# Performance work log

Measured on AMD Instinct MI355X. Metric: run time of the kernel, lower is better.

The kernel has to match this reference:

```python
import jax, jax.numpy as jnp
import numpy as np

B, T, C, H = 2, 1024, 1024, 16
N = C // H
D_W, D_A, D_V, D_G = 64, 64, 32, 160
VOCAB = 50257


def setup_inputs() -> dict:
    key = jax.random.key(0)
    ks = iter(jax.random.split(key, 48))
    rn = lambda shape, s=1.0: jax.random.normal(next(ks), shape, dtype=jnp.float32) * s
    inp = {
        'residual': rn((B, T, C)),
        'x': rn((B, T, C)),
        'v_first': rn((B, T, C)),
        'x0': rn((B, T, C)),
        'dx0': rn((B, T, C)),
        'token_ids': jax.random.randint(next(ks), (B, T), 0, VOCAB),
        # token-shift mix coefficients (1,1,C), in [0,1) like the 1-pow(ddd,...) init
        'mr': jax.random.uniform(next(ks), (1, 1, C)),
        'mw': jax.random.uniform(next(ks), (1, 1, C)),
        'mk': jax.random.uniform(next(ks), (1, 1, C)),
        'mv': jax.random.uniform(next(ks), (1, 1, C)),
        'ma': jax.random.uniform(next(ks), (1, 1, C)),
        'mg': jax.random.uniform(next(ks), (1, 1, C)),
        # decay LoRA
        'w0': rn((1, 1, C), 1.0) - 1.0,
        'w1': rn((C, D_W), 0.05),
        'w2': rn((D_W, C), 0.05),
        # in-context-learning-rate LoRA
        'a0': rn((1, 1, C), 0.3),
        'a1': rn((C, D_A), 0.05),
        'a2': rn((D_A, C), 0.05),
        # value-residual LoRA
        'v0': rn((1, 1, C), 0.3) + 0.73,
        'v1': rn((C, D_V), 0.05),
        'v2': rn((D_V, C), 0.05),
        # gate LoRA
        'g1': rn((C, D_G), 0.05),
        'g2': rn((D_G, C), 0.05),
        'k_k': rn((1, 1, C), 0.1) + 0.71,
        'k_a': rn((1, 1, C), 0.1) + 1.02,
        'r_k': rn((H, N), 0.1) - 0.04,
        # projections stored as (in, out); y = x @ W (== torch Linear with W.T)
        'W_r': rn((C, C), C ** -0.5),
        'W_k': rn((C, C), 0.1 * C ** -0.5),
        'W_v': rn((C, C), C ** -0.5),
        'W_o': rn((C, C), C ** -0.5),
        'ln_w': jnp.full((C,), ((1 + 12) / 24) ** 0.7, dtype=jnp.float32),
        'ln_b': jnp.zeros((C,), dtype=jnp.float32),
    }
    return inp


def rwkv7_scan(r, log_w, k, v, a, b):
    # all inputs [B,T,H,N]; recurrence per head on state S [N_v, N_k]:
    #   S_t = S_{t-1} * diag(exp(log_w_t)) + S_{t-1} @ (a_t b_t^T) + v_t k_t^T
    #   o_t = S_t @ r_t
    def step(S, inp):
        r_t, w_t, k_t, v_t, a_t, b_t = inp  # each [B,H,N]
        Sa = jnp.einsum('bhvk,bhk->bhv', S, a_t)
        S = (S * jnp.exp(w_t)[:, :, None, :]
             + Sa[..., None] * b_t[:, :, None, :]
             + v_t[..., None] * k_t[:, :, None, :])
        o = jnp.einsum('bhvk,bhk->bhv', S, r_t)
        return S, o

    to_t = lambda z: jnp.moveaxis(z, 1, 0)  # [T,B,H,N]
    S0 = jnp.zeros((r.shape[0], H, N, N), dtype=r.dtype)
    _, o = jax.lax.scan(step, S0, (to_t(r), to_t(log_w), to_t(k), to_t(v), to_t(a), to_t(b)))
    return jnp.moveaxis(o, 0, 1)  # [B,T,H,N]


def group_norm(x, w, b, eps=0.00064):
    # GroupNorm(H, C): normalize each head's N channels per (B,T) position
    Bx, Tx, Cx = x.shape
    xg = x.reshape(Bx, Tx, H, N)
    mu = xg.mean(-1, keepdims=True)
    var = xg.var(-1, keepdims=True)
    xg = (xg - mu) * jax.lax.rsqrt(var + eps)
    return xg.reshape(Bx, Tx, Cx) * w + b


def reference(residual, x, v_first, x0, dx0, token_ids,
              mr, mw, mk, mv, ma, mg,
              w0, w1, w2, a0, a1, a2, v0, v1, v2, g1, g2,
              k_k, k_a, r_k, W_r, W_k, W_v, W_o, ln_w, ln_b):
    Bx, Tx, Cx = x.shape
    # token shift: x_{t-1} - x_t (zero-pad first step)
    xx = jnp.pad(x, ((0, 0), (1, 0), (0, 0)))[:, :Tx] - x
    xr, xw, xk, xv, xa, xg = (x + xx * m for m in (mr, mw, mk, mv, ma, mg))

    r = xr @ W_r
    log_neglog_w = -jax.nn.softplus(-(w0 + jnp.tanh(xw @ w1) @ w2)) - 0.5
    log_w = -jnp.exp(log_neglog_w)  # in (-e^{-0.5}, 0)
    k = xk @ W_k
    v = xv @ W_v
    v = v + (v_first - v) * jax.nn.sigmoid(v0 + (xv @ v1) @ v2)
    a = jax.nn.sigmoid(a0 + (xa @ a1) @ a2)
    g = jax.nn.sigmoid(xg @ g1) @ g2

    kk = (k * k_k).reshape(Bx, Tx, H, N)
    kk = kk / jnp.maximum(jnp.linalg.norm(kk, axis=-1, keepdims=True), 1e-12)
    k = k * (1 + (a - 1) * k_a)

    r4 = r.reshape(Bx, Tx, H, N)
    w4 = log_w.reshape(Bx, Tx, H, N)
    k4 = k.reshape(Bx, Tx, H, N)
    v4 = v.reshape(Bx, Tx, H, N)
    aa = -kk
    bb = kk * a.reshape(Bx, Tx, H, N)

    o = rwkv7_scan(r4, w4, k4, v4, aa, bb)  # [B,T,H,N]
    y = group_norm(o.reshape(Bx, Tx, Cx), ln_w, ln_b)
    y = y + ((r4 * k4 * r_k).sum(-1, keepdims=True) * v4).reshape(Bx, Tx, Cx)
    y = (y * g) @ W_o
    return residual + y
```

## Files before the change

### kernel.cpp

```cpp
#include <hip/hip_runtime.h>
#include <math.h>

#define B_DIM 2
#define T_SEQ 1024
#define C_DIM 1024
#define H_DIM 16
#define N_DIM 64
#define M_ROWS (B_DIM * T_SEQ)

#define GBM 64
#define GBN 64
#define GBK 64
#define LDK 88
#define SW(r, c) ((c) ^ (((((r) >> 3) & 3)) << 3))
#define SW16(r, c) ((c) ^ ((((r) >> 3) & 1) << 4))

typedef __attribute__((ext_vector_type(8))) short bf16x8;
typedef __attribute__((ext_vector_type(4))) float f32x4;
typedef unsigned short ushortx4 __attribute__((ext_vector_type(4)));
typedef unsigned short ushortx8 __attribute__((ext_vector_type(8)));

__device__ __forceinline__ unsigned short f2bf(float f) {
    unsigned int u = __float_as_uint(f);
    u = (u + 0x7FFFu + ((u >> 16) & 1u)) >> 16;
    return (unsigned short)u;
}
__device__ __forceinline__ float bf2f(unsigned short h) {
    return __uint_as_float(((unsigned int)h) << 16);
}
__device__ __forceinline__ float fsigmoid(float x) {
    return 1.0f / (1.0f + __expf(-x));
}
__device__ __forceinline__ float ftanh(float x) {
    const float t = __expf(-2.0f * fabsf(x));
    const float r = (1.0f - t) / (1.0f + t);
    return copysignf(r, x);
}

__device__ __forceinline__ float wred64(float v) {
#pragma unroll
    for (int m = 32; m; m >>= 1) v += __shfl_xor(v, m);
    return v;
}

__global__ __launch_bounds__(256) void premix_kernel(
    const float* __restrict__ x,
    const float* mr, const float* mk, const float* mv,
    const float* mw, const float* ma, const float* mg,
    unsigned short* xr, unsigned short* xk, unsigned short* xv,
    unsigned short* xw, unsigned short* xa, unsigned short* xg)
{
    const int g = blockIdx.x * 256 + threadIdx.x;
    const size_t base = (size_t)g * 8;
    const int row = (int)(base >> 10);
    const int col = (int)(base & 1023);
    const int t_in = row & (T_SEQ - 1);

    const float* xp = x + (size_t)row * C_DIM + col;
    float4 a0 = *(const float4*)xp;
    float4 a1 = *(const float4*)(xp + 4);
    float4 p0 = make_float4(0.f, 0.f, 0.f, 0.f), p1 = p0;
    if (t_in > 0) {
        p0 = *(const float4*)(xp - C_DIM);
        p1 = *(const float4*)(xp - C_DIM + 4);
    }
    const float d0x = p0.x - a0.x, d0y = p0.y - a0.y, d0z = p0.z - a0.z, d0w = p0.w - a0.w;
    const float d1x = p1.x - a1.x, d1y = p1.y - a1.y, d1z = p1.z - a1.z, d1w = p1.w - a1.w;

    const float* ms[6] = {mr, mk, mv, mw, ma, mg};
    unsigned short* outs[6] = {xr, xk, xv, xw, xa, xg};
#pragma unroll
    for (int i = 0; i < 6; ++i) {
        const float4 m0 = *(const float4*)(ms[i] + col);
        const float4 m1 = *(const float4*)(ms[i] + col + 4);
        ushortx8 o;
        o[0] = f2bf(fmaf(d0x, m0.x, a0.x));
        o[1] = f2bf(fmaf(d0y, m0.y, a0.y));
        o[2] = f2bf(fmaf(d0z, m0.z, a0.z));
        o[3] = f2bf(fmaf(d0w, m0.w, a0.w));
        o[4] = f2bf(fmaf(d1x, m1.x, a1.x));
        o[5] = f2bf(fmaf(d1y, m1.y, a1.y));
        o[6] = f2bf(fmaf(d1z, m1.z, a1.z));
        o[7] = f2bf(fmaf(d1w, m1.w, a1.w));
        *(ushortx8*)(outs[i] + base) = o;
    }
}

__global__ __launch_bounds__(256) void wtrans_kernel(
    const float* __restrict__ W, unsigned short* __restrict__ WT)
{
    __shared__ float tile[32][33];
    const int tx = threadIdx.x, ty = threadIdx.y;
    const int n0 = blockIdx.x * 32, k0 = blockIdx.y * 32;
#pragma unroll
    for (int i = 0; i < 4; ++i)
        tile[ty + i * 8][tx] = W[(size_t)(k0 + ty + i * 8) * 1024 + n0 + tx];
    __syncthreads();
#pragma unroll
    for (int i = 0; i < 4; ++i)
        WT[(size_t)(n0 + ty + i * 8) * 1024 + k0 + tx] = f2bf(tile[tx][ty + i * 8]);
}

__global__ __launch_bounds__(256) void trans_all_kernel(
    const float* Wk, const float* Wv, const float* Wr,
    const float* w1p, const float* a1p, const float* v1p, const float* g1p,
    const float* a2p, const float* v2p, const float* g2p, const float* w2p,
    unsigned short* wtA, unsigned short* wtB, unsigned short* wtC,
    unsigned short* wt_w1, unsigned short* wt_a1, unsigned short* wt_v1,
    unsigned short* wt_g1, unsigned short* wt_a2, unsigned short* wt_v2,
    unsigned short* wt_g2, unsigned short* wt_w2)
{
    __shared__ float tile[32][33];
    const int bid = blockIdx.x;
    const float* W; unsigned short* WT; int K, N, t0;
    if      (bid < 1024) { W = Wk;  WT = wtA;   K = 1024; N = 1024; t0 = 0;    }
    else if (bid < 2048) { W = Wv;  WT = wtB;   K = 1024; N = 1024; t0 = 1024; }
    else if (bid < 3072) { W = Wr;  WT = wtC;   K = 1024; N = 1024; t0 = 2048; }
    else if (bid < 3136) { W = w1p; WT = wt_w1; K = 1024; N = 64;   t0 = 3072; }
    else if (bid < 3200) { W = a1p; WT = wt_a1; K = 1024; N = 64;   t0 = 3136; }
    else if (bid < 3232) { W = v1p; WT = wt_v1; K = 1024; N = 32;   t0 = 3200; }
    else if (bid < 3392) { W = g1p; WT = wt_g1; K = 1024; N = 160;  t0 = 3232; }
    else if (bid < 3456) { W = a2p; WT = wt_a2; K = 64;   N = 1024; t0 = 3392; }
    else if (bid < 3488) { W = v2p; WT = wt_v2; K = 32;   N = 1024; t0 = 3456; }
    else if (bid < 3648) { W = g2p; WT = wt_g2; K = 160;  N = 1024; t0 = 3488; }
    else                 { W = w2p; WT = wt_w2; K = 64;   N = 1024; t0 = 3648; }
    const int lt = bid - t0;
    const int ntx = N >> 5;
    const int n0 = (lt % ntx) * 32;
    const int k0 = (lt / ntx) * 32;
    const int tx = threadIdx.x, ty = threadIdx.y;
#pragma unroll
    for (int i = 0; i < 4; ++i)
        tile[ty + i * 8][tx] = W[(size_t)(k0 + ty + i * 8) * N + n0 + tx];
    __syncthreads();
#pragma unroll
    for (int i = 0; i < 4; ++i)
        WT[(size_t)(n0 + ty + i * 8) * K + k0 + tx] = f2bf(tile[tx][ty + i * 8]);
}

__device__ __forceinline__ void gemm_core(
    unsigned short (*As)[LDK], unsigned short (*Bs)[LDK],
    const unsigned short* __restrict__ Aarr, int arow_stride,
    const unsigned short* __restrict__ WT, int K, int Nc, int bn0, int bm0,
    unsigned short* outp, int ostr, int ooff,
    unsigned short* outh, int hoff, int post)
{
    const int tid = threadIdx.x;
    const int lane = tid & 63;
    const int wid = tid >> 6;
    const int wr = wid >> 1, wc = wid & 1;
    const int l15 = lane & 15, l4 = lane >> 4;

    const int ar = tid >> 2;
    const int as = (tid & 3) << 4;
    const int row = bm0 + ar;
    const int brn = tid >> 2;
    const int bks = (tid & 3) << 4;
    const bool bn_ok = (bn0 + brn) < Nc;

    const int ra0 = wr * 32 + l15, ra1 = wr * 32 + 16 + l15;
    const int rb0 = wc * 32 + l15, rb1 = wc * 32 + 16 + l15;

    f32x4 acc[2][2] = {};

    for (int k0 = 0; k0 < K; k0 += GBK) {
#pragma unroll
        for (int i = 0; i < 2; ++i) {
            const int kk = as + 8 * i;
            ushortx8 av = {0, 0, 0, 0, 0, 0, 0, 0};
            if (k0 + kk < K)
                av = *(const ushortx8*)(Aarr + (size_t)row * arow_stride + k0 + kk);
            *(ushortx8*)&As[ar][SW(ar, kk)] = av;
        }
#pragma unroll
        for (int i = 0; i < 2; ++i) {
            const int kk = bks + 8 * i;
            ushortx8 bv = {0, 0, 0, 0, 0, 0, 0, 0};
            if (bn_ok && (k0 + kk < K))
                bv = *(const ushortx8*)(WT + (size_t)(bn0 + brn) * K + k0 + kk);
            *(ushortx8*)&Bs[brn][SW(brn, kk)] = bv;
        }
        __syncthreads();
#pragma unroll
        for (int ks = 0; ks < 2; ++ks) {
            const int cc = ks * 32 + l4 * 8;
            bf16x8 af0 = *(const bf16x8*)&As[ra0][SW(ra0, cc)];
            bf16x8 af1 = *(const bf16x8*)&As[ra1][SW(ra1, cc)];
            bf16x8 bg0 = *(const bf16x8*)&Bs[rb0][SW(rb0, cc)];
            bf16x8 bg1 = *(const bf16x8*)&Bs[rb1][SW(rb1, cc)];
            acc[0][0] = __builtin_amdgcn_mfma_f32_16x16x32_bf16(af0, bg0, acc[0][0], 0, 0, 0);
            acc[0][1] = __builtin_amdgcn_mfma_f32_16x16x32_bf16(af0, bg1, acc[0][1], 0, 0, 0);
            acc[1][0] = __builtin_amdgcn_mfma_f32_16x16x32_bf16(af1, bg0, acc[1][0], 0, 0, 0);
            acc[1][1] = __builtin_amdgcn_mfma_f32_16x16x32_bf16(af1, bg1, acc[1][1], 0, 0, 0);
        }
        __syncthreads();
    }

#pragma unroll
    for (int fi = 0; fi < 2; ++fi)
#pragma unroll
        for (int fj = 0; fj < 2; ++fj) {
            const int ocol = bn0 + wc * 32 + fj * 16 + l15;
            if (ocol < Nc) {
#pragma unroll
                for (int p = 0; p < 4; ++p) {
                    const int orow = bm0 + wr * 32 + fi * 16 + l4 * 4 + p;
                    float v = acc[fi][fj][p];
                    if (post == 1) v = ftanh(v);
                    else if (post == 2) v = fsigmoid(v);
                    if (outh)
                        outh[(size_t)orow * 320 + hoff + ocol] = f2bf(v);
                    else
                        outp[((size_t)orow * 1024 + ocol) * ostr + ooff] = f2bf(v);
                }
            }
        }
}

__device__ __forceinline__ void gemm128_core(
    const unsigned short* __restrict__ A,
    const unsigned short* __restrict__ WT,
    int bm0, int bn0,
    unsigned short (*As)[40], unsigned short (*Bs)[40],
    f32x4 (*acc)[4])
{
    const int tid = threadIdx.x;
    const int lane = tid & 63;
    const int w = tid >> 6;
    const int wr = w >> 1, wc = w & 1;
    const int l15 = lane & 15, l4 = lane >> 4;
    const int sr = tid >> 1;
    const int sc = (tid & 1) << 4;
    const int ssc = SW16(sr, sc);

    const unsigned short* ap = A + (size_t)(bm0 + sr) * 1024 + sc;
    const unsigned short* bp = WT + (size_t)(bn0 + sr) * 1024 + sc;

    for (int k0 = 0; k0 < 1024; k0 += 32) {
        ushortx8 av0 = *(const ushortx8*)(ap + k0);
        ushortx8 av1 = *(const ushortx8*)(ap + k0 + 8);
        ushortx8 bv0 = *(const ushortx8*)(bp + k0);
        ushortx8 bv1 = *(const ushortx8*)(bp + k0 + 8);
        *(ushortx8*)&As[sr][ssc] = av0;
        *(ushortx8*)&As[sr][ssc + 8] = av1;
        *(ushortx8*)&Bs[sr][ssc] = bv0;
        *(ushortx8*)&Bs[sr][ssc + 8] = bv1;
        __syncthreads();
        bf16x8 af[4], bg[4];
#pragma unroll
        for (int f = 0; f < 4; ++f) {
            const int ra = wr * 64 + f * 16 + l15;
            const int rb = wc * 64 + f * 16 + l15;
            af[f] = *(const bf16x8*)&As[ra][SW16(ra, l4 * 8)];
            bg[f] = *(const bf16x8*)&Bs[rb][SW16(rb, l4 * 8)];
        }
#pragma unroll
        for (int fi = 0; fi < 4; ++fi)
#pragma unroll
            for (int fj = 0; fj < 4; ++fj)
                acc[fi][fj] = __builtin_amdgcn_mfma_f32_16x16x32_bf16(
                    af[fi], bg[fj], acc[fi][fj], 0, 0, 0);
        __syncthreads();
    }
}

__global__ __launch_bounds__(256) void gemm_s1_kernel(
    const unsigned short* xr, const unsigned short* xk, const unsigned short* xv,
    const unsigned short* xw, const unsigned short* xa, const unsigned short* xg,
    const unsigned short* wtA, const unsigned short* wtB, const unsigned short* wtC,
    const unsigned short* wt_a1, const unsigned short* wt_v1,
    const unsigned short* wt_g1, const unsigned short* wt_w1,
    unsigned short* b_r, unsigned short* pk_bf, unsigned short* b_v,
    unsigned short* h_cat)
{
    __shared__ __align__(16) char sarena[22528];
    const int bid = blockIdx.x;
    if (bid < 384) {
        unsigned short (*As)[40] = (unsigned short (*)[40])sarena;
        unsigned short (*Bs)[40] = (unsigned short (*)[40])(sarena + 10240);
        const int g = bid >> 7;
        const int sub = bid & 127;
        const int bn0 = (sub & 7) * 128;
        const int bm0 = (sub >> 3) * 128;
        const unsigned short* A = (g == 0) ? xr : (g == 1) ? xk : xv;
        const unsigned short* WT = (g == 0) ? wtC : (g == 1) ? wtA : wtB;

        f32x4 acc[4][4] = {};
        gemm128_core(A, WT, bm0, bn0, As, Bs, acc);

        const int lane = threadIdx.x & 63;
        const int w = threadIdx.x >> 6;
        const int wr = w >> 1, wc = w & 1;
        const int l15 = lane & 15, l4 = lane >> 4;
#pragma unroll
        for (int fi = 0; fi < 4; ++fi)
#pragma unroll
            for (int fj = 0; fj < 4; ++fj) {
                const int ocol = bn0 + wc * 64 + fj * 16 + l15;
#pragma unroll
                for (int p = 0; p < 4; ++p) {
                    const int orow = bm0 + wr * 64 + fi * 16 + l4 * 4 + p;
                    const unsigned short hv = f2bf(acc[fi][fj][p]);
                    if (g == 0) b_r[(size_t)orow * 1024 + ocol] = hv;
                    else if (g == 1) pk_bf[((size_t)orow * 1024 + ocol) * 4 + 1] = hv;
                    else b_v[(size_t)orow * 1024 + ocol] = hv;
                }
            }
    } else {
        unsigned short (*As)[LDK] = (unsigned short (*)[LDK])sarena;
        unsigned short (*Bs)[LDK] = (unsigned short (*)[LDK])(sarena + 11264);
        const int sid = bid - 384;
        const int nt = sid % 6;
        const int bm0 = (sid / 6) * 64;
        const unsigned short* A; const unsigned short* WT;
        int Nc, nb = 0, hoff, post = 0;
        if (nt == 0)      { A = xa; WT = wt_a1; hoff = 0;   Nc = 64; }
        else if (nt == 1) { A = xv; WT = wt_v1; hoff = 64;  Nc = 32; }
        else if (nt < 5)  { A = xg; WT = wt_g1; hoff = 96;  Nc = 160; nb = nt - 2; post = 2; }
        else              { A = xw; WT = wt_w1; hoff = 256; Nc = 64; post = 1; }
        gemm_core(As, Bs, A, 1024, WT, 1024, Nc, nb * 64, bm0,
                  nullptr, 1, 0, h_cat, hoff, post);
    }
}

__global__ __launch_bounds__(256) void gemm_s2_kernel(
    const unsigned short* __restrict__ h_cat,
    const unsigned short* wt_a2, const unsigned short* wt_v2,
    const unsigned short* wt_g2, const unsigned short* wt_w2,
    unsigned short* pk_bf, unsigned short* b_g)
{
    __shared__ unsigned short As[GBM][LDK];
    __shared__ unsigned short Bs[GBN][LDK];
    const int g = blockIdx.x >> 4;
    const int nb = blockIdx.x & 15;
    const int bm0 = blockIdx.y * GBM;
    const unsigned short* WT;
    unsigned short* outp; int K, aoff, ostr, ooff;
    if      (g == 0) { WT = wt_a2; K = 64;  aoff = 0;   outp = pk_bf; ostr = 4; ooff = 2; }
    else if (g == 1) { WT = wt_v2; K = 32;  aoff = 64;  outp = pk_bf; ostr = 4; ooff = 3; }
    else if (g == 2) { WT = wt_g2; K = 160; aoff = 96;  outp = b_g;   ostr = 1; ooff = 0; }
    else             { WT = wt_w2; K = 64;  aoff = 256; outp = pk_bf; ostr = 4; ooff = 0; }
    gemm_core(As, Bs, h_cat + aoff, 320, WT, K, 1024, nb * 64, bm0,
              outp, ostr, ooff, nullptr, 0, 0);
}

__global__ __launch_bounds__(256) void gemm_final128_kernel(
    const unsigned short* __restrict__ Y, const unsigned short* __restrict__ WT,
    const float* __restrict__ addend, float* __restrict__ out)
{
    __shared__ unsigned short As[128][40];
    __shared__ unsigned short Bs[128][40];
    const int bn0 = blockIdx.x * 128;
    const int bm0 = blockIdx.y * 128;

    f32x4 acc[4][4] = {};
    gemm128_core(Y, WT, bm0, bn0, As, Bs, acc);

    const int lane = threadIdx.x & 63;
    const int w = threadIdx.x >> 6;
    const int wr = w >> 1, wc = w & 1;
    const int l15 = lane & 15, l4 = lane >> 4;
#pragma unroll
    for (int fi = 0; fi < 4; ++fi)
#pragma unroll
        for (int fj = 0; fj < 4; ++fj) {
            const int ocol = bn0 + wc * 64 + fj * 16 + l15;
#pragma unroll
            for (int p = 0; p < 4; ++p) {
                const int orow = bm0 + wr * 64 + fi * 16 + l4 * 4 + p;
                out[(size_t)orow * 1024 + ocol] =
                    acc[fi][fj][p] + addend[(size_t)orow * 1024 + ocol];
            }
        }
}

__global__ __launch_bounds__(256) void chunk_prep_kernel(
    const unsigned short* __restrict__ pk_bf,
    const unsigned short* __restrict__ b_r,
    unsigned short* __restrict__ b_v,
    const float* __restrict__ v_first,
    const float* w0, const float* a0, const float* v0,
    const float* k_k, const float* k_a, const float* r_k,
    float* __restrict__ TB,
    unsigned short* __restrict__ Gt, unsigned short* __restrict__ LRt,
    float* __restrict__ Vc, float* __restrict__ Wl,
    unsigned short* __restrict__ Oi)
{
    __shared__ __align__(16) char smem[52608];
    unsigned short (*tB)[72]  = (unsigned short (*)[72])(smem + 0);
    unsigned short (*tK)[72]  = (unsigned short (*)[72])(smem + 4608);
    unsigned short (*tR)[72]  = (unsigned short (*)[72])(smem + 9216);
    unsigned short (*tBT)[40] = (unsigned short (*)[40])(smem + 13824);
    unsigned short (*VlT)[40] = (unsigned short (*)[40])(smem + 18944);
    unsigned short (*egT)[40] = (unsigned short (*)[40])(smem + 24064);
    float (*W32s)[66]         = (float (*)[66])(smem + 26624);
    float (*cg)[33]           = (float (*)[33])(smem + 26624);
    float (*dg)[33]           = (float (*)[33])(smem + 30848);
    unsigned short (*DhB)[40] = (unsigned short (*)[40])(smem + 26624);
    unsigned short (*fT)[40]  = (unsigned short (*)[40])(smem + 30848);
    float (*fg)[33]           = (float (*)[33])(smem + 35072);
    unsigned short (*tA)[72]  = (unsigned short (*)[72])(smem + 39296);
    unsigned short (*ZB)[40]  = (unsigned short (*)[40])(smem + 39296);
    float* EWZ                = (float*)(smem + 43904);
    unsigned short (*KtT)[40] = (unsigned short (*)[40])(smem + 43904);
    float* w31s               = (float*)(smem + 52352);

    const int tid = threadIdx.x;
    const int lane = tid & 63;
    const int w = tid >> 6;
    const int l15 = lane & 15, l4 = lane >> 4;
    const int bhc = blockIdx.x;
    const int bh = bhc >> 5, ck = bhc & 31;
    const int b = bh >> 4, h = bh & 15;
    const int cglob = h * 64 + lane;

    const float kkc = k_k[cglob], kac = k_a[cglob];
    const float a0c = a0[cglob], v0c = v0[cglob];
    const float w0c = w0[cglob], rkc = r_k[cglob];
#pragma unroll
    for (int q = 0; q < 8; ++q) {
        const int tq = w * 8 + q;
        const int row = b * 1024 + ck * 32 + tq;
        const size_t gi = (size_t)row * 1024 + cglob;
        const ushortx4 pk = *(const ushortx4*)(pk_bf + gi * 4);
        const float kl = bf2f(pk.y);
        const float kkv = kl * kkc;
        const float ss = wred64(kkv * kkv);
        const float kkn = kkv / fmaxf(sqrtf(ss), 1e-12f);
        const float a = fsigmoid(a0c + bf2f(pk.z));
        const float u = w0c + bf2f(pk.x);
        const float lnw = -__logf(1.0f + __expf(-u)) - 0.5f;
        const float ew = __expf(-__expf(lnw));
        const float sv = fsigmoid(v0c + bf2f(pk.w));
        const float vl = bf2f(b_v[gi]);
        const float v = fmaf(v_first[gi] - vl, sv, vl);
        const float ko = kl * (1.0f + (a - 1.0f) * kac);
        const unsigned short rbf = b_r[gi];
        const float r1f = bf2f(rbf);
        const unsigned short vbf = f2bf(v);
        b_v[gi] = vbf;

        const float t3 = wred64(r1f * ko * rkc);
        if (lane == 0) TB[bh * 1024 + ck * 32 + tq] = t3;

        EWZ[tq * 64 + lane] = ew;
        tA[tq][lane] = f2bf(-kkn);
        tB[tq][lane] = f2bf(kkn * a);
        tK[tq][lane] = f2bf(ko);
        tR[tq][lane] = rbf;
        VlT[lane][tq] = vbf;
    }
    __syncthreads();

    if (w == 0) {
        float run = 1.0f;
        for (int t = 0; t < 32; ++t) {
            run *= EWZ[t * 64 + lane];
            W32s[t][lane] = run;
        }
    }
    __syncthreads();

#pragma unroll
    for (int q = 0; q < 8; ++q) {
        const int tq = w * 8 + q;
        const float Wt = W32s[tq][lane];
        const float Wm1 = tq ? W32s[tq - 1][lane] : 1.0f;
        const float iw = 1.0f / Wt;
        tA[tq][lane] = f2bf(bf2f(tA[tq][lane]) * Wm1);
        const unsigned short tb = f2bf(bf2f(tB[tq][lane]) * iw);
        tB[tq][lane] = tb;
        tBT[lane][tq] = tb;
        tK[tq][lane] = f2bf(bf2f(tK[tq][lane]) * iw);
        tR[tq][lane] = f2bf(bf2f(tR[tq][lane]) * Wt);
    }
    if (tid < 64) w31s[tid] = W32s[31][tid];
    __syncthreads();

    {
        const unsigned short (*Am)[72] = (w == 0 || w == 2) ? tB : tK;
        const unsigned short (*Bm)[72] = (w < 2) ? tA : tR;
        f32x4 gacc[2][2] = {};
#pragma unroll
        for (int kh = 0; kh < 2; ++kh) {
            const int cc = kh * 32 + l4 * 8;
            bf16x8 ax0 = *(const bf16x8*)&Am[l15][cc];
            bf16x8 ax1 = *(const bf16x8*)&Am[16 + l15][cc];
            bf16x8 bx0 = *(const bf16x8*)&Bm[l15][cc];
            bf16x8 bx1 = *(const bf16x8*)&Bm[16 + l15][cc];
            gacc[0][0] = __builtin_amdgcn_mfma_f32_16x16x32_bf16(ax0, bx0, gacc[0][0], 0, 0, 0);
            gacc[0][1] = __builtin_amdgcn_mfma_f32_16x16x32_bf16(ax0, bx1, gacc[0][1], 0, 0, 0);
            gacc[1][0] = __builtin_amdgcn_mfma_f32_16x16x32_bf16(ax1, bx0, gacc[1][0], 0, 0, 0);
            gacc[1][1] = __builtin_amdgcn_mfma_f32_16x16x32_bf16(ax1, bx1, gacc[1][1], 0, 0, 0);
        }
#pragma unroll
        for (int mt = 0; mt < 2; ++mt)
#pragma unroll
            for (int nt = 0; nt < 2; ++nt) {
                const int col = nt * 16 + l15;
                if (w == 2) {
                    ushortx4 st;
#pragma unroll
                    for (int p = 0; p < 4; ++p) st[p] = f2bf(gacc[mt][nt][p]);
                    *(ushortx4*)&egT[col][mt * 16 + l4 * 4] = st;
                } else {
#pragma unroll
                    for (int p = 0; p < 4; ++p) {
                        const int rw = mt * 16 + l4 * 4 + p;
                        if (w == 0) cg[rw][col] = gacc[mt][nt][p];
                        else if (w == 1) dg[rw][col] = gacc[mt][nt][p];
                        else fg[rw][col] = gacc[mt][nt][p];
                    }
                }
            }
    }
    __syncthreads();

#pragma unroll
    for (int p = 0; p < 4; ++p) {
        const int idx = tid * 4 + p;
        const int r_ = idx >> 5, c_ = idx & 31;
        if (r_ >= c_) cg[r_][c_] = 0.0f;
        if (c_ <= r_) dg[r_][c_] = 0.0f;
        if (r_ > c_) fg[r_][c_] = 0.0f;
        if (c_ > r_) egT[r_][c_] = 0;
    }
    __syncthreads();

    if (w == 0) {
        for (int i = 0; i < 32; ++i) {
            float val = bf2f(tA[i][lane]);
            for (int j = 0; j < i; ++j) val += cg[j][i] * EWZ[lane * 33 + j];
            EWZ[lane * 33 + i] = val;
        }
    } else if (w == 1 && lane < 32) {
        for (int t = 0; t < 32; ++t) {
            float val = dg[lane][t];
            for (int j = 0; j < t; ++j) val += cg[j][t] * dg[lane][j];
            dg[lane][t] = val;
        }
    }
    __syncthreads();

#pragma unroll
    for (int p = 0; p < 4; ++p) {
        const int idx = tid * 4 + p;
        DhB[idx >> 5][idx & 31] = f2bf(dg[idx >> 5][idx & 31]);
    }
#pragma unroll
    for (int p = 0; p < 8; ++p) {
        const int idx = tid * 8 + p;
        ZB[idx >> 5][idx & 31] = f2bf(EWZ[(idx >> 5) * 33 + (idx & 31)]);
    }
    __syncthreads();

    const size_t cb2048 = (size_t)bhc * 2048;
    const size_t cb4096 = (size_t)bhc * 4096;

    if (w == 0) {
#pragma unroll
        for (int mt = 0; mt < 2; ++mt)
#pragma unroll
            for (int nt = 0; nt < 2; ++nt) {
                f32x4 cacc;
#pragma unroll
                for (int p = 0; p < 4; ++p) cacc[p] = fg[mt * 16 + l4 * 4 + p][nt * 16 + l15];
                bf16x8 ax = *(const bf16x8*)&DhB[mt * 16 + l15][l4 * 8];
                bf16x8 bx = *(const bf16x8*)&egT[nt * 16 + l15][l4 * 8];
                cacc = __builtin_amdgcn_mfma_f32_16x16x32_bf16(ax, bx, cacc, 0, 0, 0);
                ushortx4 st;
#pragma unroll
                for (int p = 0; p < 4; ++p) st[p] = f2bf(cacc[p]);
                *(ushortx4*)&fT[nt * 16 + l15][mt * 16 + l4 * 4] = st;
            }
    } else if (w == 1) {
#pragma unroll
        for (int mt = 0; mt < 2; ++mt)
#pragma unroll
            for (int nt = 0; nt < 4; ++nt) {
                bf16x8 ax = *(const bf16x8*)&DhB[mt * 16 + l15][l4 * 8];
                bf16x8 bx = *(const bf16x8*)&tBT[nt * 16 + l15][l4 * 8];
                f32x4 cacc = {};
                cacc = __builtin_amdgcn_mfma_f32_16x16x32_bf16(ax, bx, cacc, 0, 0, 0);
                const int col = nt * 16 + l15;
                const float w31c = w31s[col];
                ushortx4 st;
#pragma unroll
                for (int p = 0; p < 4; ++p) {
                    const int rw = mt * 16 + l4 * 4 + p;
                    st[p] = f2bf((cacc[p] + bf2f(tK[rw][col])) * w31c);
                }
                *(ushortx4*)&KtT[col][mt * 16 + l4 * 4] = st;
            }
    } else if (w == 2) {
#pragma unroll
        for (int mt = 0; mt < 4; ++mt)
#pragma unroll
            for (int nt = 0; nt < 4; ++nt) {
                bf16x8 ax = *(const bf16x8*)&tBT[mt * 16 + l15][l4 * 8];
                bf16x8 bx = *(const bf16x8*)&ZB[nt * 16 + l15][l4 * 8];
                f32x4 cacc = {};
                cacc = __builtin_amdgcn_mfma_f32_16x16x32_bf16(ax, bx, cacc, 0, 0, 0);
                const int kcol = nt * 16 + l15;
#pragma unroll
                for (int p = 0; p < 4; ++p) {
                    const int n_ = mt * 16 + l4 * 4 + p;
                    LRt[cb4096 + n_ * 64 + kcol] = f2bf(cacc[p] * w31s[n_]);
                }
            }
    } else {
#pragma unroll
        for (int mt = 0; mt < 2; ++mt)
#pragma unroll
            for (int nt = 0; nt < 4; ++nt) {
                bf16x8 ax = *(const bf16x8*)&egT[mt * 16 + l15][l4 * 8];
                bf16x8 bx = *(const bf16x8*)&ZB[nt * 16 + l15][l4 * 8];
                f32x4 cacc = {};
                cacc = __builtin_amdgcn_mfma_f32_16x16x32_bf16(ax, bx, cacc, 0, 0, 0);
                const int ncol = nt * 16 + l15;
#pragma unroll
                for (int p = 0; p < 4; ++p) {
                    const int t_ = mt * 16 + l4 * 4 + p;
                    Gt[cb2048 + t_ * 64 + ncol] = f2bf(cacc[p] + bf2f(tR[t_][ncol]));
                }
            }
    }
    __syncthreads();

    if (w < 2) {
#pragma unroll
        for (int mt = 0; mt < 2; ++mt)
#pragma unroll
            for (int ntl = 0; ntl < 2; ++ntl) {
                const int nt = w * 2 + ntl;
                bf16x8 ax = *(const bf16x8*)&fT[mt * 16 + l15][l4 * 8];
                bf16x8 bx = *(const bf16x8*)&VlT[nt * 16 + l15][l4 * 8];
                f32x4 cacc = {};
                cacc = __builtin_amdgcn_mfma_f32_16x16x32_bf16(ax, bx, cacc, 0, 0, 0);
                const int vcol = nt * 16 + l15;
#pragma unroll
                for (int p = 0; p < 4; ++p) {
                    const int t_ = mt * 16 + l4 * 4 + p;
                    Oi[cb2048 + t_ * 64 + vcol] = f2bf(cacc[p]);
                }
            }
    } else {
#pragma unroll
        for (int mtl = 0; mtl < 2; ++mtl)
#pragma unroll
            for (int nt = 0; nt < 4; ++nt) {
                const int mt = (w - 2) * 2 + mtl;
                bf16x8 ax = *(const bf16x8*)&VlT[mt * 16 + l15][l4 * 8];
                bf16x8 bx = *(const bf16x8*)&KtT[nt * 16 + l15][l4 * 8];
                f32x4 cacc = {};
                cacc = __builtin_amdgcn_mfma_f32_16x16x32_bf16(ax, bx, cacc, 0, 0, 0);
                const int ncol = nt * 16 + l15;
                float4 st = make_float4(cacc[0], cacc[1], cacc[2], cacc[3]);
                *(float4*)&Vc[cb4096 + (size_t)ncol * 64 + mt * 16 + l4 * 4] = st;
            }
    }
    if (tid < 64) Wl[(size_t)bhc * 64 + tid] = w31s[tid];
}

struct SeqRegs {
    bf16x8 g[4];
    bf16x8 lr[8];
    float4 vc[4];
    float wl[4];
    ushortx4 oi[2];
};

__device__ __forceinline__ void load_chunk(
    SeqRegs& R,
    const unsigned short* __restrict__ gt, const unsigned short* __restrict__ lr,
    const float* __restrict__ vct, const float* __restrict__ wlp,
    const unsigned short* __restrict__ oi, int l15, int l4, int vg)
{
#pragma unroll
    for (int tt = 0; tt < 2; ++tt) {
        R.g[tt * 2 + 0] = *(const bf16x8*)&gt[(tt * 16 + l15) * 64 + l4 * 8];
        R.g[tt * 2 + 1] = *(const bf16x8*)&gt[(tt * 16 + l15) * 64 + 32 + l4 * 8];
        R.oi[tt] = *(const ushortx4*)&oi[(tt * 16 + l15) * 64 + vg * 16 + l4 * 4];
    }
#pragma unroll
    for (int nt = 0; nt < 4; ++nt) {
        R.lr[nt * 2 + 0] = *(const bf16x8*)&lr[(nt * 16 + l15) * 64 + l4 * 8];
        R.lr[nt * 2 + 1] = *(const bf16x8*)&lr[(nt * 16 + l15) * 64 + 32 + l4 * 8];
        R.vc[nt] = *(const float4*)&vct[(nt * 16 + l15) * 64 + vg * 16 + l4 * 4];
        R.wl[nt] = wlp[nt * 16 + l15];
    }
}

__device__ __forceinline__ void seq_step(
    f32x4* sC, const SeqRegs& R, unsigned short (*Sst)[80],
    unsigned short* __restrict__ o, int b, int h, int c, int vg, int l15, int l4)
{
#pragma unroll
    for (int nt = 0; nt < 4; ++nt)
#pragma unroll
        for (int p = 0; p < 4; ++p)
            Sst[l4 * 4 + p][nt * 16 + l15] = f2bf(sC[nt][p]);
    __builtin_amdgcn_wave_barrier();
    bf16x8 a0 = *(const bf16x8*)&Sst[l15][l4 * 8];
    bf16x8 a1 = *(const bf16x8*)&Sst[l15][32 + l4 * 8];
    __builtin_amdgcn_wave_barrier();

    f32x4 oacc[2] = {};
#pragma unroll
    for (int tt = 0; tt < 2; ++tt) {
        oacc[tt] = __builtin_amdgcn_mfma_f32_16x16x32_bf16(a0, R.g[tt * 2 + 0], oacc[tt], 0, 0, 0);
        oacc[tt] = __builtin_amdgcn_mfma_f32_16x16x32_bf16(a1, R.g[tt * 2 + 1], oacc[tt], 0, 0, 0);
    }
    f32x4 lac[4] = {};
#pragma unroll
    for (int nt = 0; nt < 4; ++nt) {
        lac[nt] = __builtin_amdgcn_mfma_f32_16x16x32_bf16(a0, R.lr[nt * 2 + 0], lac[nt], 0, 0, 0);
        lac[nt] = __builtin_amdgcn_mfma_f32_16x16x32_bf16(a1, R.lr[nt * 2 + 1], lac[nt], 0, 0, 0);
    }

#pragma unroll
    for (int nt = 0; nt < 4; ++nt) {
        const float wlv = R.wl[nt];
#pragma unroll
        for (int p = 0; p < 4; ++p)
            sC[nt][p] = sC[nt][p] * wlv + lac[nt][p] + R.vc[nt][p];
    }

#pragma unroll
    for (int tt = 0; tt < 2; ++tt) {
        const int trow = b * 1024 + c * 32 + tt * 16 + l15;
        ushortx4 ov;
        ov.x = f2bf(oacc[tt][0] + bf2f(R.oi[tt].x));
        ov.y = f2bf(oacc[tt][1] + bf2f(R.oi[tt].y));
        ov.z = f2bf(oacc[tt][2] + bf2f(R.oi[tt].z));
        ov.w = f2bf(oacc[tt][3] + bf2f(R.oi[tt].w));
        *(ushortx4*)(o + (size_t)trow * 1024 + h * 64 + vg * 16 + l4 * 4) = ov;
    }
}

__global__ __launch_bounds__(64) void chunk_seq_kernel(
    const unsigned short* __restrict__ Gt, const unsigned short* __restrict__ LRt,
    const float* __restrict__ VcT, const float* __restrict__ Wl,
    const unsigned short* __restrict__ Oi, unsigned short* __restrict__ o)
{
    __shared__ unsigned short Sst[16][80];
    const int lane = threadIdx.x & 63;
    const int bid = blockIdx.x;
    const int bh = bid >> 2, vg = bid & 3;
    const int b = bh >> 4, h = bh & 15;
    const int l15 = lane & 15, l4 = lane >> 4;

    const size_t cbase = (size_t)bh * 32;
    const unsigned short* gt = Gt + cbase * 2048;
    const unsigned short* lr = LRt + cbase * 4096;
    const float* vct = VcT + cbase * 4096;
    const float* wlp = Wl + cbase * 64;
    const unsigned short* oi = Oi + cbase * 2048;

    f32x4 sC[4] = {};
    SeqRegs RA, RB;
    load_chunk(RA, gt, lr, vct, wlp, oi, l15, l4, vg);

    for (int cc = 0; cc < 16; ++cc) {
        const int c0 = cc * 2, c1 = cc * 2 + 1;
        load_chunk(RB, gt + (size_t)c1 * 2048, lr + (size_t)c1 * 4096,
                   vct + (size_t)c1 * 4096, wlp + (size_t)c1 * 64,
                   oi + (size_t)c1 * 2048, l15, l4, vg);
        seq_step(sC, RA, Sst, o, b, h, c0, vg, l15, l4);
        const int c2 = (c1 + 1 < 32) ? c1 + 1 : 31;
        load_chunk(RA, gt + (size_t)c2 * 2048, lr + (size_t)c2 * 4096,
                   vct + (size_t)c2 * 4096, wlp + (size_t)c2 * 64,
                   oi + (size_t)c2 * 2048, l15, l4, vg);
        seq_step(sC, RB, Sst, o, b, h, c1, vg, l15, l4);
    }
}

__global__ __launch_bounds__(256) void post_kernel(
    const unsigned short* o, const unsigned short* v, const unsigned short* g,
    const float* __restrict__ TB,
    const float* ln_w, const float* ln_b,
    unsigned short* y)
{
    const int gw = (blockIdx.x * blockDim.x + threadIdx.x) >> 6;
    const int lane = threadIdx.x & 63;
    const int row = gw >> 4;
    const int h = gw & 15;
    const int c = h * N_DIM + lane;
    const size_t idx = (size_t)row * C_DIM + c;
    const int b = row >> 10;
    const int t = row & 1023;

    const float oo = bf2f(o[idx]);
    float s1 = oo, s2 = oo * oo;
#pragma unroll
    for (int m = 32; m; m >>= 1) {
        s1 += __shfl_xor(s1, m);
        s2 += __shfl_xor(s2, m);
    }
    const float mu = s1 * (1.0f / 64.0f);
    const float var = s2 * (1.0f / 64.0f) - mu * mu;
    float yv = (oo - mu) * rsqrtf(var + 0.00064f);
    yv = yv * ln_w[c] + ln_b[c];

    yv += TB[(b * 16 + h) * 1024 + t] * bf2f(v[idx]);
    y[idx] = f2bf(yv * bf2f(g[idx]));
}

extern "C" void kernel_launch(void* const* d_in, const int* in_sizes, int n_in,
                              void* d_out, int out_size, void* d_ws, size_t ws_size,
                              hipStream_t stream) {
    (void)in_sizes; (void)n_in; (void)out_size; (void)ws_size;

    const float* residual = (const float*)d_in[0];
    const float* x        = (const float*)d_in[1];
    const float* v_first  = (const float*)d_in[2];
    const float* mr = (const float*)d_in[6];
    const float* mw = (const float*)d_in[7];
    const float* mk = (const float*)d_in[8];
    const float* mv = (const float*)d_in[9];
    const float* ma = (const float*)d_in[10];
    const float* mg = (const float*)d_in[11];
    const float* w0 = (const float*)d_in[12];
    const float* w1 = (const float*)d_in[13];
    const float* w2 = (const float*)d_in[14];
    const float* a0 = (const float*)d_in[15];
    const float* a1 = (const float*)d_in[16];
    const float* a2 = (const float*)d_in[17];
    const float* v0 = (const float*)d_in[18];
    const float* v1 = (const float*)d_in[19];
    const float* v2 = (const float*)d_in[20];
    const float* g1 = (const float*)d_in[21];
    const float* g2 = (const float*)d_in[22];
    const float* k_k = (const float*)d_in[23];
    const float* k_a = (const float*)d_in[24];
    const float* r_k = (const float*)d_in[25];
    const float* W_r = (const float*)d_in[26];
    const float* W_k = (const float*)d_in[27];
    const float* W_v = (const float*)d_in[28];
    const float* W_o = (const float*)d_in[29];
    const float* ln_w = (const float*)d_in[30];
    const float* ln_b = (const float*)d_in[31];

    float* out = (float*)d_out;
    char* wsb = (char*)d_ws;

    unsigned short* xr = (unsigned short*)(wsb + 0);
    unsigned short* xk = (unsigned short*)(wsb + 4194304);
    unsigned short* xv = (unsigned short*)(wsb + 8388608);
    unsigned short* xw = (unsigned short*)(wsb + 12582912);
    unsigned short* xa = (unsigned short*)(wsb + 16777216);
    unsigned short* xg = (unsigned short*)(wsb + 20971520);
    float* Vc          = (float*)(wsb + 0);
    unsigned short* Gt = (unsigned short*)(wsb + 16777216);
    unsigned short* Oi = (unsigned short*)(wsb + 20971520);
    unsigned short* pk_bf = (unsigned short*)(wsb + 25165824);
    unsigned short* wtD = (unsigned short*)(wsb + 25165824);
    unsigned short* y_bf = (unsigned short*)(wsb + 27262976);
    unsigned short* b_r = (unsigned short*)(wsb + 41943040);
    unsigned short* b_v = (unsigned short*)(wsb + 46137344);
    unsigned short* b_o = (unsigned short*)(wsb + 50331648);
    unsigned short* b_g = (unsigned short*)(wsb + 54525952);
    unsigned short* h_cat = (unsigned short*)(wsb + 58720256);
    unsigned short* wt_a1 = (unsigned short*)(wsb + 60293120);
    unsigned short* wt_v1 = (unsigned short*)(wsb + 60424192);
    unsigned short* wt_g1 = (unsigned short*)(wsb + 60489728);
    unsigned short* wt_a2 = (unsigned short*)(wsb + 60817408);
    unsigned short* wt_v2 = (unsigned short*)(wsb + 60948480);
    unsigned short* wt_g2 = (unsigned short*)(wsb + 61014016);
    unsigned short* wt_w1 = (unsigned short*)(wsb + 61341696);
    unsigned short* wt_w2 = (unsigned short*)(wsb + 61472768);
    unsigned short* wtA = (unsigned short*)(wsb + 61603840);
    unsigned short* wtB = (unsigned short*)(wsb + 63700992);
    unsigned short* wtC = (unsigned short*)(wsb + 65798144);
    unsigned short* LRt = (unsigned short*)(wsb + 60030976);
    float* Wl = (float*)(wsb + 68419584);
    float* TB = (float*)(wsb + 68681728);

    const dim3 blk(256);
    const dim3 tblk(32, 8);

    premix_kernel<<<dim3(1024), blk, 0, stream>>>(
        x, mr, mk, mv, mw, ma, mg, xr, xk, xv, xw, xa, xg);

    trans_all_kernel<<<dim3(3712), tblk, 0, stream>>>(
        W_k, W_v, W_r, w1, a1, v1, g1, a2, v2, g2, w2,
        wtA, wtB, wtC, wt_w1, wt_a1, wt_v1, wt_g1, wt_a2, wt_v2, wt_g2, wt_w2);

    gemm_s1_kernel<<<dim3(576), blk, 0, stream>>>(
        xr, xk, xv, xw, xa, xg, wtA, wtB, wtC,
        wt_a1, wt_v1, wt_g1, wt_w1, b_r, pk_bf, b_v, h_cat);

    gemm_s2_kernel<<<dim3(64, 32), blk, 0, stream>>>(
        h_cat, wt_a2, wt_v2, wt_g2, wt_w2, pk_bf, b_g);

    chunk_prep_kernel<<<dim3(1024), blk, 0, stream>>>(
        pk_bf, b_r, b_v, v_first, w0, a0, v0, k_k, k_a, r_k,
        TB, Gt, LRt, Vc, Wl, Oi);

    wtrans_kernel<<<dim3(32, 32), tblk, 0, stream>>>(W_o, wtD);

    chunk_seq_kernel<<<dim3(128), dim3(64), 0, stream>>>(Gt, LRt, Vc, Wl, Oi, b_o);

    post_kernel<<<dim3(8192), blk, 0, stream>>>(
        b_o, b_v, b_g, TB, ln_w, ln_b, y_bf);

    gemm_final128_kernel<<<dim3(8, 16), blk, 0, stream>>>(y_bf, wtD, residual, out);
}
```

Before: 172.7 us.

## Prefetch next GEMM K-tile into registers and split packed bf16 buffer

Both GEMM cores now issue the global loads for the next K-tile into registers right after the shared-memory barrier. This lets global memory latency overlap with the MFMA work on the current tile. The interleaved pk_bf buffer, written with a 4-element stride, is replaced by four planar bf16 arrays, so the GEMM epilogues store contiguously and chunk_prep reads them separately. The cost is extra register pressure from the prefetch registers, and four read streams instead of one vector load in chunk_prep.

```diff
diff --git a/kernel.cpp b/kernel.cpp
--- a/kernel.cpp
+++ b/kernel.cpp
@@ -142,8 +142,7 @@
     unsigned short (*As)[LDK], unsigned short (*Bs)[LDK],
     const unsigned short* __restrict__ Aarr, int arow_stride,
     const unsigned short* __restrict__ WT, int K, int Nc, int bn0, int bm0,
-    unsigned short* outp, int ostr, int ooff,
-    unsigned short* outh, int hoff, int post)
+    unsigned short* outp, unsigned short* outh, int hoff, int post)
 {
     const int tid = threadIdx.x;
     const int lane = tid & 63;
@@ -162,25 +161,34 @@
     const int rb0 = wc * 32 + l15, rb1 = wc * 32 + 16 + l15;
 
     f32x4 acc[2][2] = {};
+    const ushortx8 zz = {0, 0, 0, 0, 0, 0, 0, 0};
+    ushortx8 pa0 = zz, pa1 = zz, pb0 = zz, pb1 = zz;
+
+    if (as < K)      pa0 = *(const ushortx8*)(Aarr + (size_t)row * arow_stride + as);
+    if (as + 8 < K)  pa1 = *(const ushortx8*)(Aarr + (size_t)row * arow_stride + as + 8);
+    if (bn_ok && bks < K)     pb0 = *(const ushortx8*)(WT + (size_t)(bn0 + brn) * K + bks);
+    if (bn_ok && bks + 8 < K) pb1 = *(const ushortx8*)(WT + (size_t)(bn0 + brn) * K + bks + 8);
 
     for (int k0 = 0; k0 < K; k0 += GBK) {
-#pragma unroll
-        for (int i = 0; i < 2; ++i) {
-            const int kk = as + 8 * i;
-            ushortx8 av = {0, 0, 0, 0, 0, 0, 0, 0};
-            if (k0 + kk < K)
-                av = *(const ushortx8*)(Aarr + (size_t)row * arow_stride + k0 + kk);
-            *(ushortx8*)&As[ar][SW(ar, kk)] = av;
+        *(ushortx8*)&As[ar][SW(ar, as)] = pa0;
+        *(ushortx8*)&As[ar][SW(ar, as + 8)] = pa1;
+        *(ushortx8*)&Bs[brn][SW(brn, bks)] = pb0;
+        *(ushortx8*)&Bs[brn][SW(brn, bks + 8)] = pb1;
+        __syncthreads();
+
+        const int kn = k0 + GBK;
+        if (kn < K) {
+            pa0 = zz; pa1 = zz; pb0 = zz; pb1 = zz;
+            if (kn + as < K)
+                pa0 = *(const ushortx8*)(Aarr + (size_t)row * arow_stride + kn + as);
+            if (kn + as + 8 < K)
+                pa1 = *(const ushortx8*)(Aarr + (size_t)row * arow_stride + kn + as + 8);
+            if (bn_ok && kn + bks < K)
+                pb0 = *(const ushortx8*)(WT + (size_t)(bn0 + brn) * K + kn + bks);
+            if (bn_ok && kn + bks + 8 < K)
+                pb1 = *(const ushortx8*)(WT + (size_t)(bn0 + brn) * K + kn + bks + 8);
         }
-#pragma unroll
-        for (int i = 0; i < 2; ++i) {
-            const int kk = bks + 8 * i;
-            ushortx8 bv = {0, 0, 0, 0, 0, 0, 0, 0};
-            if (bn_ok && (k0 + kk < K))
-                bv = *(const ushortx8*)(WT + (size_t)(bn0 + brn) * K + k0 + kk);
-            *(ushortx8*)&Bs[brn][SW(brn, kk)] = bv;
-        }
-        __syncthreads();
+
 #pragma unroll
         for (int ks = 0; ks < 2; ++ks) {
             const int cc = ks * 32 + l4 * 8;
@@ -211,7 +219,7 @@
                     if (outh)
                         outh[(size_t)orow * 320 + hoff + ocol] = f2bf(v);
                     else
-                        outp[((size_t)orow * 1024 + ocol) * ostr + ooff] = f2bf(v);
+                        outp[(size_t)orow * 1024 + ocol] = f2bf(v);
                 }
             }
         }
@@ -236,16 +244,24 @@
     const unsigned short* ap = A + (size_t)(bm0 + sr) * 1024 + sc;
     const unsigned short* bp = WT + (size_t)(bn0 + sr) * 1024 + sc;
 
+    ushortx8 av0 = *(const ushortx8*)(ap);
+    ushortx8 av1 = *(const ushortx8*)(ap + 8);
+    ushortx8 bv0 = *(const ushortx8*)(bp);
+    ushortx8 bv1 = *(const ushortx8*)(bp + 8);
+
     for (int k0 = 0; k0 < 1024; k0 += 32) {
-        ushortx8 av0 = *(const ushortx8*)(ap + k0);
-        ushortx8 av1 = *(const ushortx8*)(ap + k0 + 8);
-        ushortx8 bv0 = *(const ushortx8*)(bp + k0);
-        ushortx8 bv1 = *(const ushortx8*)(bp + k0 + 8);
         *(ushortx8*)&As[sr][ssc] = av0;
         *(ushortx8*)&As[sr][ssc + 8] = av1;
         *(ushortx8*)&Bs[sr][ssc] = bv0;
         *(ushortx8*)&Bs[sr][ssc + 8] = bv1;
         __syncthreads();
+
+        const int kn = (k0 + 32 < 1024) ? k0 + 32 : k0;
+        av0 = *(const ushortx8*)(ap + kn);
+        av1 = *(const ushortx8*)(ap + kn + 8);
+        bv0 = *(const ushortx8*)(bp + kn);
+        bv1 = *(const ushortx8*)(bp + kn + 8);
+
         bf16x8 af[4], bg[4];
 #pragma unroll
         for (int f = 0; f < 4; ++f) {
@@ -270,7 +286,7 @@
     const unsigned short* wtA, const unsigned short* wtB, const unsigned short* wtC,
     const unsigned short* wt_a1, const unsigned short* wt_v1,
     const unsigned short* wt_g1, const unsigned short* wt_w1,
-    unsigned short* b_r, unsigned short* pk_bf, unsigned short* b_v,
+    unsigned short* b_r, unsigned short* b_k, unsigned short* b_v,
     unsigned short* h_cat)
 {
     __shared__ __align__(16) char sarena[22528];
@@ -284,6 +300,7 @@
         const int bm0 = (sub >> 3) * 128;
         const unsigned short* A = (g == 0) ? xr : (g == 1) ? xk : xv;
         const unsigned short* WT = (g == 0) ? wtC : (g == 1) ? wtA : wtB;
+        unsigned short* O = (g == 0) ? b_r : (g == 1) ? b_k : b_v;
 
         f32x4 acc[4][4] = {};
         gemm128_core(A, WT, bm0, bn0, As, Bs, acc);
@@ -300,10 +317,7 @@
 #pragma unroll
                 for (int p = 0; p < 4; ++p) {
                     const int orow = bm0 + wr * 64 + fi * 16 + l4 * 4 + p;
-                    const unsigned short hv = f2bf(acc[fi][fj][p]);
-                    if (g == 0) b_r[(size_t)orow * 1024 + ocol] = hv;
-                    else if (g == 1) pk_bf[((size_t)orow * 1024 + ocol) * 4 + 1] = hv;
-                    else b_v[(size_t)orow * 1024 + ocol] = hv;
+                    O[(size_t)orow * 1024 + ocol] = f2bf(acc[fi][fj][p]);
                 }
             }
     } else {
@@ -319,7 +333,7 @@
         else if (nt < 5)  { A = xg; WT = wt_g1; hoff = 96;  Nc = 160; nb = nt - 2; post = 2; }
         else              { A = xw; WT = wt_w1; hoff = 256; Nc = 64; post = 1; }
         gemm_core(As, Bs, A, 1024, WT, 1024, Nc, nb * 64, bm0,
-                  nullptr, 1, 0, h_cat, hoff, post);
+                  nullptr, h_cat, hoff, post);
     }
 }
 
@@ -327,7 +341,8 @@
     const unsigned short* __restrict__ h_cat,
     const unsigned short* wt_a2, const unsigned short* wt_v2,
     const unsigned short* wt_g2, const unsigned short* wt_w2,
-    unsigned short* pk_bf, unsigned short* b_g)
+    unsigned short* b_a, unsigned short* b_vg, unsigned short* b_g,
+    unsigned short* b_wl)
 {
     __shared__ unsigned short As[GBM][LDK];
     __shared__ unsigned short Bs[GBN][LDK];
@@ -335,13 +350,13 @@
     const int nb = blockIdx.x & 15;
     const int bm0 = blockIdx.y * GBM;
     const unsigned short* WT;
-    unsigned short* outp; int K, aoff, ostr, ooff;
-    if      (g == 0) { WT = wt_a2; K = 64;  aoff = 0;   outp = pk_bf; ostr = 4; ooff = 2; }
-    else if (g == 1) { WT = wt_v2; K = 32;  aoff = 64;  outp = pk_bf; ostr = 4; ooff = 3; }
-    else if (g == 2) { WT = wt_g2; K = 160; aoff = 96;  outp = b_g;   ostr = 1; ooff = 0; }
-    else             { WT = wt_w2; K = 64;  aoff = 256; outp = pk_bf; ostr = 4; ooff = 0; }
+    unsigned short* outp; int K, aoff;
+    if      (g == 0) { WT = wt_a2; K = 64;  aoff = 0;   outp = b_a; }
+    else if (g == 1) { WT = wt_v2; K = 32;  aoff = 64;  outp = b_vg; }
+    else if (g == 2) { WT = wt_g2; K = 160; aoff = 96;  outp = b_g; }
+    else             { WT = wt_w2; K = 64;  aoff = 256; outp = b_wl; }
     gemm_core(As, Bs, h_cat + aoff, 320, WT, K, 1024, nb * 64, bm0,
-              outp, ostr, ooff, nullptr, 0, 0);
+              outp, nullptr, 0, 0);
 }
 
 __global__ __launch_bounds__(256) void gemm_final128_kernel(
@@ -375,7 +390,8 @@
 }
 
 __global__ __launch_bounds__(256) void chunk_prep_kernel(
-    const unsigned short* __restrict__ pk_bf,
+    const unsigned short* __restrict__ b_wl, const unsigned short* __restrict__ b_k,
+    const unsigned short* __restrict__ b_a, const unsigned short* __restrict__ b_vg,
     const unsigned short* __restrict__ b_r,
     unsigned short* __restrict__ b_v,
     const float* __restrict__ v_first,
@@ -422,16 +438,15 @@
         const int tq = w * 8 + q;
         const int row = b * 1024 + ck * 32 + tq;
         const size_t gi = (size_t)row * 1024 + cglob;
-        const ushortx4 pk = *(const ushortx4*)(pk_bf + gi * 4);
-        const float kl = bf2f(pk.y);
+        const float kl = bf2f(b_k[gi]);
         const float kkv = kl * kkc;
         const float ss = wred64(kkv * kkv);
         const float kkn = kkv / fmaxf(sqrtf(ss), 1e-12f);
-        const float a = fsigmoid(a0c + bf2f(pk.z));
-        const float u = w0c + bf2f(pk.x);
+        const float a = fsigmoid(a0c + bf2f(b_a[gi]));
+        const float u = w0c + bf2f(b_wl[gi]);
         const float lnw = -__logf(1.0f + __expf(-u)) - 0.5f;
         const float ew = __expf(-__expf(lnw));
-        const float sv = fsigmoid(v0c + bf2f(pk.w));
+        const float sv = fsigmoid(v0c + bf2f(b_vg[gi]));
         const float vl = bf2f(b_v[gi]);
         const float v = fmaf(v_first[gi] - vl, sv, vl);
         const float ko = kl * (1.0f + (a - 1.0f) * kac);
@@ -853,8 +868,11 @@
     float* Vc          = (float*)(wsb + 0);
     unsigned short* Gt = (unsigned short*)(wsb + 16777216);
     unsigned short* Oi = (unsigned short*)(wsb + 20971520);
-    unsigned short* pk_bf = (unsigned short*)(wsb + 25165824);
-    unsigned short* wtD = (unsigned short*)(wsb + 25165824);
+    unsigned short* b_wl = (unsigned short*)(wsb + 25165824);
+    unsigned short* b_k  = (unsigned short*)(wsb + 29360128);
+    unsigned short* b_a  = (unsigned short*)(wsb + 33554432);
+    unsigned short* b_vg = (unsigned short*)(wsb + 37748736);
+    unsigned short* wtD  = (unsigned short*)(wsb + 25165824);
     unsigned short* y_bf = (unsigned short*)(wsb + 27262976);
     unsigned short* b_r = (unsigned short*)(wsb + 41943040);
     unsigned short* b_v = (unsigned short*)(wsb + 46137344);
@@ -888,13 +906,13 @@
 
     gemm_s1_kernel<<<dim3(576), blk, 0, stream>>>(
         xr, xk, xv, xw, xa, xg, wtA, wtB, wtC,
-        wt_a1, wt_v1, wt_g1, wt_w1, b_r, pk_bf, b_v, h_cat);
+        wt_a1, wt_v1, wt_g1, wt_w1, b_r, b_k, b_v, h_cat);
 
     gemm_s2_kernel<<<dim3(64, 32), blk, 0, stream>>>(
-        h_cat, wt_a2, wt_v2, wt_g2, wt_w2, pk_bf, b_g);
+        h_cat, wt_a2, wt_v2, wt_g2, wt_w2, b_a, b_vg, b_g, b_wl);
 
     chunk_prep_kernel<<<dim3(1024), blk, 0, stream>>>(
-        pk_bf, b_r, b_v, v_first, w0, a0, v0, k_k, k_a, r_k,
+        b_wl, b_k, b_a, b_vg, b_r, b_v, v_first, w0, a0, v0, k_k, k_a, r_k,
         TB, Gt, LRt, Vc, Wl, Oi);
 
     wtrans_kernel<<<dim3(32, 32), tblk, 0, stream>>>(W_o, wtD);
```

Result: faster. 155.4 us (-10.0%).
